# Performance work log

Hardware: AMD Instinct MI355X
Metric: run time of the kernel (lower is better)

## Reference

```python
import jax, jax.numpy as jnp
import numpy as np
import math

N_EMBD = 1024
N_HEAD = 16
B, T, T_PLAN = 2, 2048, 512
EPS = 1e-5


def _layernorm(x, g, b):
    m = jnp.mean(x, axis=-1, keepdims=True)
    v = jnp.mean(jnp.square(x - m), axis=-1, keepdims=True)
    return (x - m) * jax.lax.rsqrt(v + EPS) * g + b


def setup_inputs() -> dict:
    key = jax.random.key(0)
    ks = jax.random.split(key, 16)
    C = N_EMBD
    s = 0.02
    inp = {
        "x": jax.random.normal(ks[0], (B, T, C), jnp.float32),
        "plan_hidden": jax.random.normal(ks[1], (B, T_PLAN, C), jnp.float32),
        "ln1_g": jnp.ones((C,), jnp.float32), "ln1_b": jnp.zeros((C,), jnp.float32),
        # weights stored as [in, out] (torch Linear applies x @ W.T)
        "c_attn_w": s * jax.random.normal(ks[2], (C, 3 * C), jnp.float32),
        "c_attn_b": jnp.zeros((3 * C,), jnp.float32),
        "attn_proj_w": s * jax.random.normal(ks[3], (C, C), jnp.float32),
        "attn_proj_b": jnp.zeros((C,), jnp.float32),
        "ln2_g": jnp.ones((C,), jnp.float32), "ln2_b": jnp.zeros((C,), jnp.float32),
        "q_w": s * jax.random.normal(ks[4], (C, C), jnp.float32), "q_b": jnp.zeros((C,), jnp.float32),
        "k_w": s * jax.random.normal(ks[5], (C, C), jnp.float32), "k_b": jnp.zeros((C,), jnp.float32),
        "v_w": s * jax.random.normal(ks[6], (C, C), jnp.float32), "v_b": jnp.zeros((C,), jnp.float32),
        "ca_proj_w": s * jax.random.normal(ks[7], (C, C), jnp.float32),
        "ca_proj_b": jnp.zeros((C,), jnp.float32),
        "ln3_g": jnp.ones((C,), jnp.float32), "ln3_b": jnp.zeros((C,), jnp.float32),
        "fc_w": s * jax.random.normal(ks[8], (C, 4 * C), jnp.float32),
        "fc_b": jnp.zeros((4 * C,), jnp.float32),
        "mlp_proj_w": s * jax.random.normal(ks[9], (4 * C, C), jnp.float32),
        "mlp_proj_b": jnp.zeros((C,), jnp.float32),
    }
    return inp


def _split_heads(t, n_head):  # [B,T,C] -> [B,H,T,D]
    Bs, Ts, Cs = t.shape
    return t.reshape(Bs, Ts, n_head, Cs // n_head).transpose(0, 2, 1, 3)


def _merge_heads(t):  # [B,H,T,D] -> [B,T,C]
    Bs, H, Ts, D = t.shape
    return t.transpose(0, 2, 1, 3).reshape(Bs, Ts, H * D)


def _self_attn(x, c_attn_w, c_attn_b, proj_w, proj_b):
    Bs, Ts, C = x.shape
    qkv = x @ c_attn_w + c_attn_b
    q, k, v = jnp.split(qkv, 3, axis=-1)
    q, k, v = (_split_heads(t, N_HEAD) for t in (q, k, v))
    scale = 1.0 / math.sqrt(C // N_HEAD)
    att = jnp.einsum("bhqd,bhkd->bhqk", q, k) * scale
    mask = jnp.tril(jnp.ones((Ts, Ts), bool))
    att = jnp.where(mask, att, -jnp.inf)
    att = jax.nn.softmax(att, axis=-1)
    y = jnp.einsum("bhqk,bhkd->bhqd", att, v)
    return _merge_heads(y) @ proj_w + proj_b


def _cross_attn(x, plan, q_w, q_b, k_w, k_b, v_w, v_b, proj_w, proj_b):
    C = x.shape[-1]
    q = _split_heads(x @ q_w + q_b, N_HEAD)
    k = _split_heads(plan @ k_w + k_b, N_HEAD)
    v = _split_heads(plan @ v_w + v_b, N_HEAD)
    scale = 1.0 / math.sqrt(C // N_HEAD)
    att = jax.nn.softmax(jnp.einsum("bhqd,bhkd->bhqk", q, k) * scale, axis=-1)
    y = jnp.einsum("bhqk,bhkd->bhqd", att, v)
    return _merge_heads(y) @ proj_w + proj_b


def reference(x, plan_hidden, ln1_g, ln1_b, c_attn_w, c_attn_b, attn_proj_w, attn_proj_b,
              ln2_g, ln2_b, q_w, q_b, k_w, k_b, v_w, v_b, ca_proj_w, ca_proj_b,
              ln3_g, ln3_b, fc_w, fc_b, mlp_proj_w, mlp_proj_b):
    x = x + _self_attn(_layernorm(x, ln1_g, ln1_b), c_attn_w, c_attn_b, attn_proj_w, attn_proj_b)
    x = x + _cross_attn(_layernorm(x, ln2_g, ln2_b), plan_hidden,
                        q_w, q_b, k_w, k_b, v_w, v_b, ca_proj_w, ca_proj_b)
    h = _layernorm(x, ln3_g, ln3_b)
    h = jax.nn.gelu(h @ fc_w + fc_b, approximate=False) @ mlp_proj_w + mlp_proj_b
    return x + h
```

## Files before the change

### kernel.cpp

```cpp
#include <hip/hip_runtime.h>
#include <stdint.h>

typedef __bf16 bf16;
typedef __bf16 bf16x4 __attribute__((ext_vector_type(4)));
typedef __bf16 bf16x8 __attribute__((ext_vector_type(8)));
typedef float  f32x4  __attribute__((ext_vector_type(4)));

#define DEVI __device__ __forceinline__

DEVI void gll16(const void* g, void* l) {
  __builtin_amdgcn_global_load_lds(
      (const __attribute__((address_space(1))) void*)g,
      (__attribute__((address_space(3))) void*)l,
      16, 0, 0);
}

DEVI f32x4 mfma16(bf16x8 a, bf16x8 b, f32x4 c) {
  return __builtin_amdgcn_mfma_f32_16x16x32_bf16(a, b, c, 0, 0, 0);
}

__global__ void k_conv_bf16(const float* __restrict__ in, bf16* __restrict__ out, int n4) {
  int i = blockIdx.x * 256 + threadIdx.x;
  if (i < n4) {
    f32x4 v = ((const f32x4*)in)[i];
    bf16x4 o;
    o[0] = (bf16)v[0]; o[1] = (bf16)v[1]; o[2] = (bf16)v[2]; o[3] = (bf16)v[3];
    ((bf16x4*)out)[i] = o;
  }
}

__global__ void k_concat2(const float* __restrict__ a, const float* __restrict__ b,
                          float* __restrict__ out, int n) {
  int i = blockIdx.x * 256 + threadIdx.x;
  if (i < n) out[i] = a[i];
  else if (i < 2 * n) out[i] = b[i - n];
}

__global__ void k_wt(const float* __restrict__ W, bf16* __restrict__ WT, int K, int N) {
  __shared__ float t[64][65];
  int bn = blockIdx.x * 64, bk = blockIdx.y * 64;
  int tx = threadIdx.x, ty = threadIdx.y;
#pragma unroll
  for (int i = 0; i < 16; ++i)
    t[ty + i * 4][tx] = W[(size_t)(bk + ty + i * 4) * N + bn + tx];
  __syncthreads();
#pragma unroll
  for (int i = 0; i < 16; ++i)
    WT[(size_t)(bn + ty + i * 4) * K + bk + tx] = (bf16)t[tx][ty + i * 4];
}

__global__ __launch_bounds__(256)
void k_ln(const float* __restrict__ x, const float* __restrict__ g,
          const float* __restrict__ b, bf16* __restrict__ out) {
  int row = blockIdx.x, tid = threadIdx.x;
  f32x4 v = ((const f32x4*)(x + (size_t)row * 1024))[tid];
  float s = v[0] + v[1] + v[2] + v[3];
  float sq = v[0]*v[0] + v[1]*v[1] + v[2]*v[2] + v[3]*v[3];
#pragma unroll
  for (int m = 1; m < 64; m <<= 1) {
    s  += __shfl_xor(s, m, 64);
    sq += __shfl_xor(sq, m, 64);
  }
  __shared__ float ps[4], psq[4];
  int w = tid >> 6;
  if ((tid & 63) == 0) { ps[w] = s; psq[w] = sq; }
  __syncthreads();
  s  = ps[0] + ps[1] + ps[2] + ps[3];
  sq = psq[0] + psq[1] + psq[2] + psq[3];
  float mean = s * (1.f / 1024.f);
  float rs = rsqrtf(sq * (1.f / 1024.f) - mean * mean + 1e-5f);
  f32x4 gv = ((const f32x4*)g)[tid];
  f32x4 bv = ((const f32x4*)b)[tid];
  bf16x4 o;
#pragma unroll
  for (int i = 0; i < 4; ++i) o[i] = (bf16)((v[i] - mean) * rs * gv[i] + bv[i]);
  ((bf16x4*)(out + (size_t)row * 1024))[tid] = o;
}

template <int EPI>
__global__ __launch_bounds__(256, 3)
void k_gemm_s(const bf16* __restrict__ A, const bf16* __restrict__ BT,
              const float* __restrict__ bias, void* __restrict__ Cout,
              int M, int N, int K, const float* __restrict__ Xres) {
  __shared__ __align__(16) char SA[2][8192];
  __shared__ __align__(16) char SB[2][16384];
  const int tid = threadIdx.x;
  const int lane = tid & 63;
  const int w = tid >> 6;
  const int wr = w >> 1, wc = w & 1;
  const int lr = lane & 15, lg = lane >> 4;
  const int nk = K >> 6;

  const int nwg = gridDim.x;
  const int q = nwg >> 3, r = nwg & 7;
  const int xcd = blockIdx.x & 7, loc = blockIdx.x >> 3;
  const int wg = (xcd < r ? xcd * (q + 1) : r * (q + 1) + (xcd - r) * q) + loc;
  const int gy = M >> 6;
  const int m0 = (wg % gy) << 6, n0 = (wg / gy) << 7;

  const int c8 = tid & 7;
  const int hrb = tid >> 3;
  auto stgA = [&](int buf, int ktc) {
#pragma unroll
    for (int i = 0; i < 2; ++i) {
      int hr = i * 32 + hrb;
      const bf16* s = A + (size_t)(m0 + hr) * K + ((size_t)ktc << 6) + ((c8 ^ (hr & 7)) << 3);
      gll16(s, &SA[buf][(i * 256 + tid) * 16]);
    }
  };
  auto stgB = [&](int buf, int ktc) {
#pragma unroll
    for (int i = 0; i < 4; ++i) {
      int hr = i * 32 + hrb;
      const bf16* s = BT + (size_t)(n0 + hr) * K + ((size_t)ktc << 6) + ((c8 ^ (hr & 7)) << 3);
      gll16(s, &SB[buf][(i * 256 + tid) * 16]);
    }
  };
  auto rdf = [&](const char* base, int rloc, int ks) -> bf16x8 {
    return *(const bf16x8*)(base + rloc * 128 + (((ks << 6) + (lg << 4)) ^ ((rloc & 7) << 4)));
  };

  f32x4 acc[2][4] = {};

  stgA(0, 0); stgB(0, 0);
  __syncthreads();
  for (int kt = 0; kt < nk; ++kt) {
    const int cur = kt & 1;
    if (kt + 1 < nk) { stgA(cur ^ 1, kt + 1); stgB(cur ^ 1, kt + 1); }
    bf16x8 af[2][2], bfr[4][2];
#pragma unroll
    for (int i = 0; i < 2; ++i)
#pragma unroll
      for (int ks = 0; ks < 2; ++ks)
        af[i][ks] = rdf(SA[cur], wr * 32 + i * 16 + lr, ks);
#pragma unroll
    for (int j = 0; j < 4; ++j)
#pragma unroll
      for (int ks = 0; ks < 2; ++ks)
        bfr[j][ks] = rdf(SB[cur], wc * 64 + j * 16 + lr, ks);
#pragma unroll
    for (int i = 0; i < 2; ++i)
#pragma unroll
      for (int j = 0; j < 4; ++j)
#pragma unroll
        for (int ks = 0; ks < 2; ++ks)
          acc[i][j] = mfma16(af[i][ks], bfr[j][ks], acc[i][j]);
    __syncthreads();
  }

  float* of = (float*)Cout;
  bf16*  ob = (bf16*)Cout;
#pragma unroll
  for (int j = 0; j < 4; ++j) {
    int gn = n0 + wc * 64 + j * 16 + lr;
    float bv = bias[gn];
#pragma unroll
    for (int i = 0; i < 2; ++i) {
      int gmb = m0 + wr * 32 + i * 16 + lg * 4;
#pragma unroll
      for (int rr = 0; rr < 4; ++rr) {
        size_t idx = (size_t)(gmb + rr) * N + gn;
        float v = acc[i][j][rr] + bv;
        if (EPI == 0) ob[idx] = (bf16)v;
        else if (EPI == 1) of[idx] += v;
        else if (EPI == 3) of[idx] = Xres[idx] + v;
        else {
          float ge = 0.5f * v * (1.f + erff(v * 0.70710678f));
          ob[idx] = (bf16)ge;
        }
      }
    }
  }
}

template <int EPI>
__global__ __launch_bounds__(512, 2)
void k_gemm8(const bf16* __restrict__ A, const bf16* __restrict__ BT,
             const float* __restrict__ bias, void* __restrict__ Cout,
             int M, int N, int K) {
  __shared__ __align__(16) char SA[2][2][16384];
  __shared__ __align__(16) char SB[2][2][16384];
  const int tid = threadIdx.x;
  const int lane = tid & 63;
  const int w = tid >> 6;
  const int wm = w >> 2, wn = w & 3;
  const int lr = lane & 15, lg = lane >> 4;
  const int nk = K >> 6;

  const int nwg = gridDim.x;
  const int q = nwg >> 3, r = nwg & 7;
  const int xcd = blockIdx.x & 7, loc = blockIdx.x >> 3;
  const int wg = (xcd < r ? xcd * (q + 1) : r * (q + 1) + (xcd - r) * q) + loc;
  const int gy = M >> 8;
  const int m0 = (wg % gy) << 8, n0 = (wg / gy) << 8;

  const int c8 = tid & 7;
  auto stg = [&](char* dst, const bf16* src0, int base0, int half, int ktc) {
#pragma unroll
    for (int i = 0; i < 2; ++i) {
      int hr = i * 64 + (tid >> 3);
      const bf16* s = src0 + (size_t)(base0 + half * 128 + hr) * K + ((size_t)ktc << 6)
                    + ((c8 ^ (hr & 7)) << 3);
      gll16(s, dst + (i * 512 + tid) * 16);
    }
  };
  auto rdf = [&](const char* hbase, int rloc, int ks) -> bf16x8 {
    return *(const bf16x8*)(hbase + rloc * 128 + (((ks << 6) + (lg << 4)) ^ ((rloc & 7) << 4)));
  };

  f32x4 acc[8][4] = {};
  bf16x8 af[4][2], b0f[2][2], b1f[2][2];

  stg(SA[0][0], A, m0, 0, 0);
  stg(SB[0][0], BT, n0, 0, 0);
  stg(SB[0][1], BT, n0, 1, 0);
  stg(SA[0][1], A, m0, 1, 0);
  stg(SA[1][0], A, m0, 0, 1);
  stg(SB[1][0], BT, n0, 0, 1);
  asm volatile("s_waitcnt vmcnt(8)" ::: "memory");
  __builtin_amdgcn_s_barrier();

  for (int kt = 0; kt < nk; ++kt) {
    const int cur = kt & 1;
    const char* hA0 = SA[cur][0]; const char* hA1 = SA[cur][1];
    const char* hB0 = SB[cur][0]; const char* hB1 = SB[cur][1];
    const int tn  = (kt + 1 < nk) ? kt + 1 : nk - 1;
    const int tn2 = (kt + 2 < nk) ? kt + 2 : nk - 1;

    stg(SB[(kt + 1) & 1][1], BT, n0, 1, tn);
    asm volatile("s_waitcnt vmcnt(8)" ::: "memory");
#pragma unroll
    for (int i = 0; i < 4; ++i) {
      int rl = i * 32 + wm * 16 + lr;
#pragma unroll
      for (int ks = 0; ks < 2; ++ks) af[i][ks] = rdf(hA0, rl, ks);
    }
#pragma unroll
    for (int j = 0; j < 2; ++j) {
      int rl = j * 64 + wn * 16 + lr;
#pragma unroll
      for (int ks = 0; ks < 2; ++ks) b0f[j][ks] = rdf(hB0, rl, ks);
    }
    __builtin_amdgcn_s_barrier();
    __builtin_amdgcn_s_setprio(1);
#pragma unroll
    for (int i = 0; i < 4; ++i)
#pragma unroll
      for (int j = 0; j < 2; ++j)
#pragma unroll
        for (int ks = 0; ks < 2; ++ks)
          acc[i][j] = mfma16(af[i][ks], b0f[j][ks], acc[i][j]);
    __builtin_amdgcn_s_setprio(0);

    stg(SA[(kt + 1) & 1][1], A, m0, 1, tn);
    asm volatile("s_waitcnt vmcnt(8)" ::: "memory");
#pragma unroll
    for (int j = 0; j < 2; ++j) {
      int rl = j * 64 + wn * 16 + lr;
#pragma unroll
      for (int ks = 0; ks < 2; ++ks) b1f[j][ks] = rdf(hB1, rl, ks);
    }
    __builtin_amdgcn_s_barrier();
    __builtin_amdgcn_s_setprio(1);
#pragma unroll
    for (int i = 0; i < 4; ++i)
#pragma unroll
      for (int j = 0; j < 2; ++j)
#pragma unroll
        for (int ks = 0; ks < 2; ++ks)
          acc[i][2 + j] = mfma16(af[i][ks], b1f[j][ks], acc[i][2 + j]);
    __builtin_amdgcn_s_setprio(0);

    stg(SA[cur][0], A, m0, 0, tn2);
#pragma unroll
    for (int i = 0; i < 4; ++i) {
      int rl = i * 32 + wm * 16 + lr;
#pragma unroll
      for (int ks = 0; ks < 2; ++ks) af[i][ks] = rdf(hA1, rl, ks);
    }
    __builtin_amdgcn_s_barrier();
    __builtin_amdgcn_s_setprio(1);
#pragma unroll
    for (int i = 0; i < 4; ++i)
#pragma unroll
      for (int j = 0; j < 2; ++j)
#pragma unroll
        for (int ks = 0; ks < 2; ++ks)
          acc[4 + i][j] = mfma16(af[i][ks], b0f[j][ks], acc[4 + i][j]);
    __builtin_amdgcn_s_setprio(0);

    stg(SB[cur][0], BT, n0, 0, tn2);
    asm volatile("s_waitcnt vmcnt(8)" ::: "memory");
    __builtin_amdgcn_s_barrier();
    __builtin_amdgcn_s_setprio(1);
#pragma unroll
    for (int i = 0; i < 4; ++i)
#pragma unroll
      for (int j = 0; j < 2; ++j)
#pragma unroll
        for (int ks = 0; ks < 2; ++ks)
          acc[4 + i][2 + j] = mfma16(af[i][ks], b1f[j][ks], acc[4 + i][2 + j]);
    __builtin_amdgcn_s_setprio(0);
  }

  float* of = (float*)Cout;
  bf16*  ob = (bf16*)Cout;
#pragma unroll
  for (int ni = 0; ni < 4; ++ni) {
    int gn = n0 + (ni >> 1) * 128 + (ni & 1) * 64 + wn * 16 + lr;
    float bv = bias[gn];
#pragma unroll
    for (int mi = 0; mi < 8; ++mi) {
      int gmb = m0 + (mi >> 2) * 128 + (mi & 3) * 32 + wm * 16 + lg * 4;
#pragma unroll
      for (int rr = 0; rr < 4; ++rr) {
        size_t idx = (size_t)(gmb + rr) * N + gn;
        float v = acc[mi][ni][rr] + bv;
        if (EPI == 0) ob[idx] = (bf16)v;
        else if (EPI == 1) of[idx] += v;
        else {
          float ge = 0.5f * v * (1.f + erff(v * 0.70710678f));
          ob[idx] = (bf16)ge;
        }
      }
    }
  }
}

template <bool CAUSAL>
__global__ __launch_bounds__(256)
void k_attn2(const bf16* __restrict__ Qb, int ldq, int qcol0,
             const bf16* __restrict__ Kb, int kcol0,
             const bf16* __restrict__ Vb, int vcol0,
             int ldkv, int qlen, int kvlen,
             bf16* __restrict__ Ob, int ldo, float scale) {
  const int tid = threadIdx.x;
  const int lane = tid & 63;
  const int w = tid >> 6;
  const int lr = lane & 15, lg = lane >> 4;

  int id = blockIdx.x;
  int h, b, qt;
  if (CAUSAL) {
    int low = id & 255;
    h = low & 15; b = (low >> 4) & 1;
    int q3 = low >> 5;
    qt = (id >> 8) ? (8 + q3) : (7 - q3);
  } else {
    h = id & 15; b = (id >> 4) & 1; qt = id >> 5;
  }

  const int qbase = qt * 128;
  const int kvbase = b * kvlen;
  const int nkv = CAUSAL ? (2 * qt + 2) : (kvlen >> 6);
  const int mask_from = CAUSAL ? (nkv - 2) : 0x7fffffff;

  bf16x8 qf[2][2];
#pragma unroll
  for (int g = 0; g < 2; ++g)
#pragma unroll
    for (int kk = 0; kk < 2; ++kk)
      qf[g][kk] = *(const bf16x8*)(Qb + (size_t)(b * qlen + qbase + w * 32 + g * 16 + lr) * ldq
                                   + qcol0 + h * 64 + kk * 32 + lg * 8);

  __shared__ __align__(16) char Klds[2][8192];
  __shared__ __align__(16) bf16 VT[2][64][68];

  f32x4 o[2][4] = {};
  float mrun[2] = {-3.0e38f, -3.0e38f};
  float lsum[2] = {0.f, 0.f};

  bf16x8 vr0, vr1;
  const int vkv = lane;
  const int vd0 = (tid >> 6) * 16;
  const bf16* Vbase = Vb + vcol0 + h * 64 + vd0;

  auto stageK = [&](int buf, int kvt) {
#pragma unroll
    for (int t = 0; t < 2; ++t) {
      int r = t * 32 + (tid >> 3);
      int pb = (tid & 7) * 16;
      const char* gs = (const char*)(Kb + (size_t)(kvbase + kvt * 64 + r) * ldkv + kcol0 + h * 64)
                       + (pb ^ ((r & 7) << 4));
      gll16(gs, &Klds[buf][t * 4096 + tid * 16]);
    }
  };
  auto loadV = [&](int kvt) {
    const bf16* vp = Vbase + (size_t)(kvbase + kvt * 64 + vkv) * ldkv;
    vr0 = *(const bf16x8*)vp;
    vr1 = *(const bf16x8*)(vp + 8);
  };
  auto writeV = [&](int buf) {
#pragma unroll
    for (int i = 0; i < 8; ++i) VT[buf][vd0 + i][vkv] = vr0[i];
#pragma unroll
    for (int i = 0; i < 8; ++i) VT[buf][vd0 + 8 + i][vkv] = vr1[i];
  };

  stageK(0, 0);
  loadV(0);
  writeV(0);
  __syncthreads();

  int cur = 0;
  for (int kvt = 0; kvt < nkv; ++kvt) {
    if (kvt + 1 < nkv) { stageK(cur ^ 1, kvt + 1); loadV(kvt + 1); }

    f32x4 s[2][4] = {};
#pragma unroll
    for (int sub = 0; sub < 4; ++sub) {
      int row = sub * 16 + lr;
#pragma unroll
      for (int kk = 0; kk < 2; ++kk) {
        bf16x8 kf = *(const bf16x8*)&Klds[cur][(row << 7) + ((kk * 64 + lg * 16) ^ ((row & 7) << 4))];
        s[0][sub] = mfma16(kf, qf[0][kk], s[0][sub]);
        s[1][sub] = mfma16(kf, qf[1][kk], s[1][sub]);
      }
    }

    const bool domask = CAUSAL && (kvt >= mask_from);
    bf16x8 pa[2][2];
#pragma unroll
    for (int g = 0; g < 2; ++g) {
      const int qg = qbase + w * 32 + g * 16 + lr;
      float pmax = -3.0e38f;
#pragma unroll
      for (int sub = 0; sub < 4; ++sub)
#pragma unroll
        for (int j = 0; j < 4; ++j) {
          float v = s[g][sub][j] * scale;
          if (domask) {
            int kvg = kvt * 64 + sub * 16 + lg * 4 + j;
            if (kvg > qg) v = -3.0e38f;
          }
          s[g][sub][j] = v;
          pmax = fmaxf(pmax, v);
        }
      pmax = fmaxf(pmax, __shfl_xor(pmax, 16, 64));
      pmax = fmaxf(pmax, __shfl_xor(pmax, 32, 64));
      float mnew = mrun[g];
      if (__any(pmax - mrun[g] > 8.f)) {
        mnew = fmaxf(mrun[g], pmax);
        float alpha = __expf(mrun[g] - mnew);
        lsum[g] *= alpha;
        float al[4];
#pragma unroll
        for (int j = 0; j < 4; ++j) {
          int src = (lane & 48) | (lg * 4 + j);
          al[j] = __int_as_float(__builtin_amdgcn_ds_bpermute(src << 2, __float_as_int(alpha)));
        }
#pragma unroll
        for (int dt = 0; dt < 4; ++dt)
#pragma unroll
          for (int j = 0; j < 4; ++j) o[g][dt][j] *= al[j];
      }
      float psum = 0.f;
#pragma unroll
      for (int sub = 0; sub < 4; ++sub)
#pragma unroll
        for (int j = 0; j < 4; ++j) {
          float p = __expf(s[g][sub][j] - mnew);
          s[g][sub][j] = p;
          psum += p;
        }
      psum += __shfl_xor(psum, 16, 64);
      psum += __shfl_xor(psum, 32, 64);
      lsum[g] += psum;
      mrun[g] = mnew;
#pragma unroll
      for (int sp = 0; sp < 2; ++sp) {
#pragma unroll
        for (int j = 0; j < 4; ++j) {
          pa[g][sp][j]     = (bf16)s[g][2 * sp][j];
          pa[g][sp][4 + j] = (bf16)s[g][2 * sp + 1][j];
        }
      }
    }

#pragma unroll
    for (int sp = 0; sp < 2; ++sp) {
#pragma unroll
      for (int dt = 0; dt < 4; ++dt) {
        int d = dt * 16 + lr;
        bf16x4 va  = *(const bf16x4*)&VT[cur][d][sp * 32 + lg * 4];
        bf16x4 vb2 = *(const bf16x4*)&VT[cur][d][sp * 32 + 16 + lg * 4];
        bf16x8 vf = __builtin_shufflevector(va, vb2, 0, 1, 2, 3, 4, 5, 6, 7);
        o[0][dt] = mfma16(pa[0][sp], vf, o[0][dt]);
        o[1][dt] = mfma16(pa[1][sp], vf, o[1][dt]);
      }
    }

    if (kvt + 1 < nkv) writeV(cur ^ 1);
    __syncthreads();
    cur ^= 1;
  }

#pragma unroll
  for (int g = 0; g < 2; ++g) {
    float il[4];
#pragma unroll
    for (int j = 0; j < 4; ++j) {
      int src = (lane & 48) | (lg * 4 + j);
      float ls = __int_as_float(__builtin_amdgcn_ds_bpermute(src << 2, __float_as_int(lsum[g])));
      il[j] = 1.0f / ls;
    }
#pragma unroll
    for (int dt = 0; dt < 4; ++dt)
#pragma unroll
      for (int j = 0; j < 4; ++j) {
        int gq = b * qlen + qbase + w * 32 + g * 16 + lg * 4 + j;
        Ob[(size_t)gq * ldo + h * 64 + dt * 16 + lr] = (bf16)(o[g][dt][j] * il[j]);
      }
  }
}

extern "C" void kernel_launch(void* const* d_in, const int* in_sizes, int n_in,
                              void* d_out, int out_size, void* d_ws, size_t ws_size,
                              hipStream_t stream) {
  (void)in_sizes; (void)n_in; (void)out_size; (void)ws_size;
  const float* x        = (const float*)d_in[0];
  const float* plan     = (const float*)d_in[1];
  const float* ln1_g    = (const float*)d_in[2];
  const float* ln1_b    = (const float*)d_in[3];
  const float* c_attn_w = (const float*)d_in[4];
  const float* c_attn_b = (const float*)d_in[5];
  const float* aproj_w  = (const float*)d_in[6];
  const float* aproj_b  = (const float*)d_in[7];
  const float* ln2_g    = (const float*)d_in[8];
  const float* ln2_b    = (const float*)d_in[9];
  const float* q_w      = (const float*)d_in[10];
  const float* q_b      = (const float*)d_in[11];
  const float* k_w      = (const float*)d_in[12];
  const float* k_b      = (const float*)d_in[13];
  const float* v_w      = (const float*)d_in[14];
  const float* v_b      = (const float*)d_in[15];
  const float* ca_w     = (const float*)d_in[16];
  const float* ca_b     = (const float*)d_in[17];
  const float* ln3_g    = (const float*)d_in[18];
  const float* ln3_b    = (const float*)d_in[19];
  const float* fc_w     = (const float*)d_in[20];
  const float* fc_b     = (const float*)d_in[21];
  const float* mp_w     = (const float*)d_in[22];
  const float* mp_b     = (const float*)d_in[23];

  char* ws = (char*)d_ws;
  bf16*  wbuf   = (bf16*)(ws);
  bf16*  lnb    = (bf16*)(ws + (8ull << 20));
  bf16*  planb  = (bf16*)(ws + (16ull << 20));
  bf16*  yb     = (bf16*)(ws + (18ull << 20));
  char*  rega   = ws + (26ull << 20);
  float* biaskv = (float*)(ws + (58ull << 20));
  bf16* qkv  = (bf16*)rega;
  bf16* qx   = (bf16*)rega;
  bf16* kvc  = (bf16*)(rega + (8ull << 20));
  bf16* hmid = (bf16*)rega;
  float* xw = (float*)d_out;

  dim3 wtb(64, 4);

  k_conv_bf16<<<1024, 256, 0, stream>>>(plan, planb, 262144);
  k_concat2<<<8, 256, 0, stream>>>(k_b, v_b, biaskv, 1024);

  k_ln<<<4096, 256, 0, stream>>>(x, ln1_g, ln1_b, lnb);
  k_wt<<<dim3(48, 16), wtb, 0, stream>>>(c_attn_w, wbuf, 1024, 3072);
  k_gemm8<0><<<192, 512, 0, stream>>>(lnb, wbuf, c_attn_b, qkv, 4096, 3072, 1024);
  k_attn2<true><<<512, 256, 0, stream>>>(qkv, 3072, 0, qkv, 1024, qkv, 2048,
                                         3072, 2048, 2048, yb, 1024, 0.125f);
  k_wt<<<dim3(16, 16), wtb, 0, stream>>>(aproj_w, wbuf, 1024, 1024);
  k_gemm_s<3><<<512, 256, 0, stream>>>(yb, wbuf, aproj_b, xw, 4096, 1024, 1024, x);

  k_ln<<<4096, 256, 0, stream>>>(xw, ln2_g, ln2_b, lnb);
  k_wt<<<dim3(16, 16), wtb, 0, stream>>>(q_w, wbuf, 1024, 1024);
  k_gemm_s<0><<<512, 256, 0, stream>>>(lnb, wbuf, q_b, qx, 4096, 1024, 1024, nullptr);
  k_wt<<<dim3(16, 16), wtb, 0, stream>>>(k_w, wbuf, 1024, 1024);
  k_wt<<<dim3(16, 16), wtb, 0, stream>>>(v_w, wbuf + 1024 * 1024, 1024, 1024);
  k_gemm_s<0><<<256, 256, 0, stream>>>(planb, wbuf, biaskv, kvc, 1024, 2048, 1024, nullptr);
  k_attn2<false><<<512, 256, 0, stream>>>(qx, 1024, 0, kvc, 0, kvc, 1024,
                                          2048, 2048, 512, yb, 1024, 0.125f);
  k_wt<<<dim3(16, 16), wtb, 0, stream>>>(ca_w, wbuf, 1024, 1024);
  k_gemm_s<1><<<512, 256, 0, stream>>>(yb, wbuf, ca_b, xw, 4096, 1024, 1024, nullptr);

  k_ln<<<4096, 256, 0, stream>>>(xw, ln3_g, ln3_b, lnb);
  k_wt<<<dim3(64, 16), wtb, 0, stream>>>(fc_w, wbuf, 1024, 4096);
  k_gemm8<2><<<256, 512, 0, stream>>>(lnb, wbuf, fc_b, hmid, 4096, 4096, 1024);
  k_wt<<<dim3(16, 64), wtb, 0, stream>>>(mp_w, wbuf, 4096, 1024);
  k_gemm_s<1><<<512, 256, 0, stream>>>(hmid, wbuf, mp_b, xw, 4096, 1024, 4096, nullptr);
}
```

Measured before the change: 361.3 us.

## Fuse weight-transpose launches into co-scheduled megakernels with LN, attention and GEMMs

Weight transpose/convert blocks are appended to the grids of adjacent independent kernels (layernorm, attention, projection GEMMs), so the transposes run alongside other work instead of as separate launches. Buffers are reassigned so each transposed weight lives in its own workspace region (q/k/v weights in rega, mlp_proj weight in yb, cross-attention output in a new region). This removes about ten kernel launches and the idle tail between them. In exchange the shared-memory arena grows to the largest body size, which can lower occupancy for the layernorm blocks, and the buffer aliasing now has to be correct.

```diff
diff --git a/kernel.cpp b/kernel.cpp
--- a/kernel.cpp
+++ b/kernel.cpp
@@ -36,10 +36,11 @@
   else if (i < 2 * n) out[i] = b[i - n];
 }
 
-__global__ void k_wt(const float* __restrict__ W, bf16* __restrict__ WT, int K, int N) {
-  __shared__ float t[64][65];
-  int bn = blockIdx.x * 64, bk = blockIdx.y * 64;
-  int tx = threadIdx.x, ty = threadIdx.y;
+DEVI void wt_body(char* arena, const float* __restrict__ W, bf16* __restrict__ WT,
+                  int K, int N, int bx, int by, int tid) {
+  float (*t)[65] = reinterpret_cast<float(*)[65]>(arena);
+  int bn = bx * 64, bk = by * 64;
+  int tx = tid & 63, ty = tid >> 6;
 #pragma unroll
   for (int i = 0; i < 16; ++i)
     t[ty + i * 4][tx] = W[(size_t)(bk + ty + i * 4) * N + bn + tx];
@@ -49,10 +50,10 @@
     WT[(size_t)(bn + ty + i * 4) * K + bk + tx] = (bf16)t[tx][ty + i * 4];
 }
 
-__global__ __launch_bounds__(256)
-void k_ln(const float* __restrict__ x, const float* __restrict__ g,
-          const float* __restrict__ b, bf16* __restrict__ out) {
-  int row = blockIdx.x, tid = threadIdx.x;
+DEVI void ln_body(char* arena, const float* __restrict__ x, const float* __restrict__ g,
+                  const float* __restrict__ b, bf16* __restrict__ out, int row, int tid) {
+  float* ps  = (float*)arena;
+  float* psq = ps + 4;
   f32x4 v = ((const f32x4*)(x + (size_t)row * 1024))[tid];
   float s = v[0] + v[1] + v[2] + v[3];
   float sq = v[0]*v[0] + v[1]*v[1] + v[2]*v[2] + v[3]*v[3];
@@ -61,7 +62,6 @@
     s  += __shfl_xor(s, m, 64);
     sq += __shfl_xor(sq, m, 64);
   }
-  __shared__ float ps[4], psq[4];
   int w = tid >> 6;
   if ((tid & 63) == 0) { ps[w] = s; psq[w] = sq; }
   __syncthreads();
@@ -77,13 +77,34 @@
   ((bf16x4*)(out + (size_t)row * 1024))[tid] = o;
 }
 
+__global__ __launch_bounds__(256)
+void k_ln(const float* __restrict__ x, const float* __restrict__ g,
+          const float* __restrict__ b, bf16* __restrict__ out) {
+  __shared__ __align__(16) char arena[64];
+  ln_body(arena, x, g, b, out, blockIdx.x, threadIdx.x);
+}
+
+__global__ __launch_bounds__(256)
+void mega_ln_wt(const float* __restrict__ x, const float* __restrict__ g,
+                const float* __restrict__ b, bf16* __restrict__ out,
+                const float* __restrict__ W, bf16* __restrict__ WT,
+                int K, int N, int wgx) {
+  __shared__ __align__(16) char arena[16640];
+  if ((int)blockIdx.x < 4096) {
+    ln_body(arena, x, g, b, out, blockIdx.x, threadIdx.x);
+  } else {
+    int wid = blockIdx.x - 4096;
+    wt_body(arena, W, WT, K, N, wid % wgx, wid / wgx, threadIdx.x);
+  }
+}
+
 template <int EPI>
-__global__ __launch_bounds__(256, 3)
-void k_gemm_s(const bf16* __restrict__ A, const bf16* __restrict__ BT,
-              const float* __restrict__ bias, void* __restrict__ Cout,
-              int M, int N, int K, const float* __restrict__ Xres) {
-  __shared__ __align__(16) char SA[2][8192];
-  __shared__ __align__(16) char SB[2][16384];
+DEVI void gemm_s_body(char* arena, const bf16* __restrict__ A, const bf16* __restrict__ BT,
+                      const float* __restrict__ bias, void* __restrict__ Cout,
+                      int M, int N, int K, const float* __restrict__ Xres,
+                      int nwg, int bid) {
+  char (*SA)[8192]  = reinterpret_cast<char(*)[8192]>(arena);
+  char (*SB)[16384] = reinterpret_cast<char(*)[16384]>(arena + 16384);
   const int tid = threadIdx.x;
   const int lane = tid & 63;
   const int w = tid >> 6;
@@ -91,9 +112,8 @@
   const int lr = lane & 15, lg = lane >> 4;
   const int nk = K >> 6;
 
-  const int nwg = gridDim.x;
   const int q = nwg >> 3, r = nwg & 7;
-  const int xcd = blockIdx.x & 7, loc = blockIdx.x >> 3;
+  const int xcd = bid & 7, loc = bid >> 3;
   const int wg = (xcd < r ? xcd * (q + 1) : r * (q + 1) + (xcd - r) * q) + loc;
   const int gy = M >> 6;
   const int m0 = (wg % gy) << 6, n0 = (wg / gy) << 7;
@@ -170,6 +190,47 @@
         }
       }
     }
+  }
+}
+
+template <int EPI>
+__global__ __launch_bounds__(256, 3)
+void k_gemm_s(const bf16* __restrict__ A, const bf16* __restrict__ BT,
+              const float* __restrict__ bias, void* __restrict__ Cout,
+              int M, int N, int K, const float* __restrict__ Xres) {
+  __shared__ __align__(16) char arena[49152];
+  gemm_s_body<EPI>(arena, A, BT, bias, Cout, M, N, K, Xres, gridDim.x, blockIdx.x);
+}
+
+__global__ __launch_bounds__(256, 3)
+void mega_gemmA2(const bf16* __restrict__ A, const bf16* __restrict__ BT,
+                 const float* __restrict__ bias, void* __restrict__ Cout,
+                 const float* __restrict__ Xres,
+                 const float* __restrict__ qw, bf16* __restrict__ qwt,
+                 const float* __restrict__ kw, bf16* __restrict__ kwt,
+                 const float* __restrict__ vw, bf16* __restrict__ vwt) {
+  __shared__ __align__(16) char arena[49152];
+  if ((int)blockIdx.x < 512) {
+    gemm_s_body<3>(arena, A, BT, bias, Cout, 4096, 1024, 1024, Xres, 512, blockIdx.x);
+  } else {
+    int wid = blockIdx.x - 512;
+    const float* W = wid < 256 ? qw : (wid < 512 ? kw : vw);
+    bf16* WT = wid < 256 ? qwt : (wid < 512 ? kwt : vwt);
+    int sub = wid & 255;
+    wt_body(arena, W, WT, 1024, 1024, sub & 15, sub >> 4, threadIdx.x);
+  }
+}
+
+__global__ __launch_bounds__(256, 3)
+void mega_gemmB2(const bf16* __restrict__ A, const bf16* __restrict__ BT,
+                 const float* __restrict__ bias, void* __restrict__ Cout,
+                 const float* __restrict__ mw, bf16* __restrict__ mwt) {
+  __shared__ __align__(16) char arena[49152];
+  if ((int)blockIdx.x < 512) {
+    gemm_s_body<1>(arena, A, BT, bias, Cout, 4096, 1024, 1024, nullptr, 512, blockIdx.x);
+  } else {
+    int wid = blockIdx.x - 512;
+    wt_body(arena, mw, mwt, 4096, 1024, wid & 15, wid >> 4, threadIdx.x);
   }
 }
 
@@ -328,18 +389,19 @@
 }
 
 template <bool CAUSAL>
-__global__ __launch_bounds__(256)
-void k_attn2(const bf16* __restrict__ Qb, int ldq, int qcol0,
-             const bf16* __restrict__ Kb, int kcol0,
-             const bf16* __restrict__ Vb, int vcol0,
-             int ldkv, int qlen, int kvlen,
-             bf16* __restrict__ Ob, int ldo, float scale) {
+DEVI void attn_body(char* arena, int id,
+                    const bf16* __restrict__ Qb, int ldq, int qcol0,
+                    const bf16* __restrict__ Kb, int kcol0,
+                    const bf16* __restrict__ Vb, int vcol0,
+                    int ldkv, int qlen, int kvlen,
+                    bf16* __restrict__ Ob, int ldo, float scale) {
+  char (*Klds)[8192]   = reinterpret_cast<char(*)[8192]>(arena);
+  bf16 (*VT)[64][68]   = reinterpret_cast<bf16(*)[64][68]>(arena + 16384);
   const int tid = threadIdx.x;
   const int lane = tid & 63;
   const int w = tid >> 6;
   const int lr = lane & 15, lg = lane >> 4;
 
-  int id = blockIdx.x;
   int h, b, qt;
   if (CAUSAL) {
     int low = id & 255;
@@ -362,9 +424,6 @@
     for (int kk = 0; kk < 2; ++kk)
       qf[g][kk] = *(const bf16x8*)(Qb + (size_t)(b * qlen + qbase + w * 32 + g * 16 + lr) * ldq
                                    + qcol0 + h * 64 + kk * 32 + lg * 8);
-
-  __shared__ __align__(16) char Klds[2][8192];
-  __shared__ __align__(16) bf16 VT[2][64][68];
 
   f32x4 o[2][4] = {};
   float mrun[2] = {-3.0e38f, -3.0e38f};
@@ -511,6 +570,24 @@
         int gq = b * qlen + qbase + w * 32 + g * 16 + lg * 4 + j;
         Ob[(size_t)gq * ldo + h * 64 + dt * 16 + lr] = (bf16)(o[g][dt][j] * il[j]);
       }
+  }
+}
+
+template <bool CAUSAL>
+__global__ __launch_bounds__(256)
+void mega_attn_wt(const bf16* __restrict__ Qb, int ldq, int qcol0,
+                  const bf16* __restrict__ Kb, int kcol0,
+                  const bf16* __restrict__ Vb, int vcol0,
+                  int ldkv, int qlen, int kvlen,
+                  bf16* __restrict__ Ob, int ldo, float scale,
+                  const float* __restrict__ W, bf16* __restrict__ WT) {
+  __shared__ __align__(16) char arena[33792];
+  if ((int)blockIdx.x < 512) {
+    attn_body<CAUSAL>(arena, blockIdx.x, Qb, ldq, qcol0, Kb, kcol0, Vb, vcol0,
+                      ldkv, qlen, kvlen, Ob, ldo, scale);
+  } else {
+    int wid = blockIdx.x - 512;
+    wt_body(arena, W, WT, 1024, 1024, wid & 15, wid >> 4, threadIdx.x);
   }
 }
 
@@ -551,38 +628,36 @@
   char*  rega   = ws + (26ull << 20);
   float* biaskv = (float*)(ws + (58ull << 20));
   bf16* qkv  = (bf16*)rega;
-  bf16* qx   = (bf16*)rega;
+  bf16* qwt  = (bf16*)rega;
+  bf16* kwt  = (bf16*)(rega + (2ull << 20));
+  bf16* vwt  = (bf16*)(rega + (4ull << 20));
   bf16* kvc  = (bf16*)(rega + (8ull << 20));
+  bf16* co   = (bf16*)(rega + (12ull << 20));
   bf16* hmid = (bf16*)rega;
   float* xw = (float*)d_out;
 
-  dim3 wtb(64, 4);
-
   k_conv_bf16<<<1024, 256, 0, stream>>>(plan, planb, 262144);
   k_concat2<<<8, 256, 0, stream>>>(k_b, v_b, biaskv, 1024);
 
-  k_ln<<<4096, 256, 0, stream>>>(x, ln1_g, ln1_b, lnb);
-  k_wt<<<dim3(48, 16), wtb, 0, stream>>>(c_attn_w, wbuf, 1024, 3072);
+  mega_ln_wt<<<4096 + 768, 256, 0, stream>>>(x, ln1_g, ln1_b, lnb,
+                                             c_attn_w, wbuf, 1024, 3072, 48);
   k_gemm8<0><<<192, 512, 0, stream>>>(lnb, wbuf, c_attn_b, qkv, 4096, 3072, 1024);
-  k_attn2<true><<<512, 256, 0, stream>>>(qkv, 3072, 0, qkv, 1024, qkv, 2048,
-                                         3072, 2048, 2048, yb, 1024, 0.125f);
-  k_wt<<<dim3(16, 16), wtb, 0, stream>>>(aproj_w, wbuf, 1024, 1024);
-  k_gemm_s<3><<<512, 256, 0, stream>>>(yb, wbuf, aproj_b, xw, 4096, 1024, 1024, x);
+  mega_attn_wt<true><<<512 + 256, 256, 0, stream>>>(qkv, 3072, 0, qkv, 1024, qkv, 2048,
+                                                    3072, 2048, 2048, yb, 1024, 0.125f,
+                                                    aproj_w, wbuf);
+  mega_gemmA2<<<512 + 768, 256, 0, stream>>>(yb, wbuf, aproj_b, xw, x,
+                                             q_w, qwt, k_w, kwt, v_w, vwt);
 
   k_ln<<<4096, 256, 0, stream>>>(xw, ln2_g, ln2_b, lnb);
-  k_wt<<<dim3(16, 16), wtb, 0, stream>>>(q_w, wbuf, 1024, 1024);
-  k_gemm_s<0><<<512, 256, 0, stream>>>(lnb, wbuf, q_b, qx, 4096, 1024, 1024, nullptr);
-  k_wt<<<dim3(16, 16), wtb, 0, stream>>>(k_w, wbuf, 1024, 1024);
-  k_wt<<<dim3(16, 16), wtb, 0, stream>>>(v_w, wbuf + 1024 * 1024, 1024, 1024);
-  k_gemm_s<0><<<256, 256, 0, stream>>>(planb, wbuf, biaskv, kvc, 1024, 2048, 1024, nullptr);
-  k_attn2<false><<<512, 256, 0, stream>>>(qx, 1024, 0, kvc, 0, kvc, 1024,
-                                          2048, 2048, 512, yb, 1024, 0.125f);
-  k_wt<<<dim3(16, 16), wtb, 0, stream>>>(ca_w, wbuf, 1024, 1024);
-  k_gemm_s<1><<<512, 256, 0, stream>>>(yb, wbuf, ca_b, xw, 4096, 1024, 1024, nullptr);
-
-  k_ln<<<4096, 256, 0, stream>>>(xw, ln3_g, ln3_b, lnb);
-  k_wt<<<dim3(64, 16), wtb, 0, stream>>>(fc_w, wbuf, 1024, 4096);
+  k_gemm_s<0><<<512, 256, 0, stream>>>(lnb, qwt, q_b, yb, 4096, 1024, 1024, nullptr);
+  k_gemm_s<0><<<256, 256, 0, stream>>>(planb, kwt, biaskv, kvc, 1024, 2048, 1024, nullptr);
+  mega_attn_wt<false><<<512 + 256, 256, 0, stream>>>(yb, 1024, 0, kvc, 0, kvc, 1024,
+                                                     2048, 2048, 512, co, 1024, 0.125f,
+                                                     ca_w, wbuf);
+  mega_gemmB2<<<512 + 1024, 256, 0, stream>>>(co, wbuf, ca_b, xw, mp_w, yb);
+
+  mega_ln_wt<<<4096 + 1024, 256, 0, stream>>>(xw, ln3_g, ln3_b, lnb,
+                                              fc_w, wbuf, 1024, 4096, 64);
   k_gemm8<2><<<256, 512, 0, stream>>>(lnb, wbuf, fc_b, hmid, 4096, 4096, 1024);
-  k_wt<<<dim3(16, 64), wtb, 0, stream>>>(mp_w, wbuf, 4096, 1024);
-  k_gemm_s<1><<<512, 256, 0, stream>>>(hmid, wbuf, mp_b, xw, 4096, 1024, 4096, nullptr);
-}
+  k_gemm_s<1><<<512, 256, 0, stream>>>(hmid, yb, mp_b, xw, 4096, 1024, 4096, nullptr);
+}
```

Result: faster. 315.6 us (-12.7%).
